# Optimization experiments

Measured on AMD Instinct MI355X. Metric: run time of the kernel, lower is better.

## Reference

```python
import jax, jax.numpy as jnp
import numpy as np

ALPHA = 2.0          # spikingjelly surrogate.ATan default alpha
V_THRESHOLD = 1.0    # IFNode default
# v_reset = 0.0 -> hard reset

@jax.custom_vjp
def atan_spike(x):
    # Heaviside forward, ATan surrogate backward
    return (x >= 0).astype(x.dtype)

def _atan_fwd(x):
    return atan_spike(x), x

def _atan_bwd(x, g):
    sg = (ALPHA / 2.0) / (1.0 + (jnp.pi / 2.0 * ALPHA * x) ** 2)
    return (g * sg,)

atan_spike.defvjp(_atan_fwd, _atan_bwd)

def if_node(x_seq):
    # x_seq: [T, B, D]; IF neuron: v += x; spike = H(v - th); hard reset to 0.
    # detach_reset=True -> stop_gradient on spike in the reset path.
    def step(v, xt):
        v = v + xt
        s = atan_spike(v - V_THRESHOLD)
        v = v * (1.0 - jax.lax.stop_gradient(s))
        return v, s
    v0 = jnp.zeros(x_seq.shape[1:], x_seq.dtype)
    _, spikes = jax.lax.scan(step, v0, x_seq)
    return spikes

def setup_inputs() -> dict:
    key = jax.random.key(0)
    k0, k1, k2, k3, k4 = jax.random.split(key, 5)
    B = 65536
    x = jax.random.normal(k0, (B, 1, 28, 28), dtype=jnp.float32)
    # Linear(28, 32) and Linear(32, 10) params (PyTorch layout: [out, in])
    W1 = jax.random.uniform(k1, (32, 28), jnp.float32, -1.0, 1.0) / np.sqrt(28.0).astype(np.float32)
    b1 = jax.random.uniform(k2, (32,), jnp.float32, -1.0, 1.0) / np.sqrt(28.0).astype(np.float32)
    W2 = jax.random.uniform(k3, (10, 32), jnp.float32, -1.0, 1.0) / np.sqrt(32.0).astype(np.float32)
    b2 = jax.random.uniform(k4, (10,), jnp.float32, -1.0, 1.0) / np.sqrt(32.0).astype(np.float32)
    return {"x": x, "W1": W1, "b1": b1, "W2": W2, "b2": b2}

def reference(x, W1, b1, W2, b2):
    # x: [B, 1, 28, 28] -> squeeze(1) -> [B, 28, 28] -> permute(2,0,1) -> [T=28, B, 28]
    xs = jnp.transpose(x[:, 0], (2, 0, 1))
    h1 = jnp.einsum('tbi,oi->tbo', xs, W1) + b1   # [28, B, 32]
    s1 = if_node(h1)
    h2 = jnp.einsum('tbi,oi->tbo', s1, W2) + b2   # [28, B, 10]
    s2 = if_node(h2)
    return s2.mean(axis=0)                         # [B, 10] firing rates
```

## Files before the change

kernel.cpp:

```cpp
#include <hip/hip_runtime.h>


#define SPB     8
#define THREADS 256

__global__ __launch_bounds__(THREADS, 4) void snn_if_kernel(
    const float* __restrict__ x,
    const float* __restrict__ W1,
    const float* __restrict__ b1,
    const float* __restrict__ W2,
    const float* __restrict__ b2,
    float* __restrict__ out,
    int B)
{
    __shared__ __align__(16) float xT[SPB][28][32];
    __shared__ float Tbl[1280];

    const int tid = threadIdx.x;
    const int o   = tid & 31;
    const int sl  = tid >> 5;
    const int S0  = blockIdx.x * SPB;
    const int nS  = (B - S0 < SPB) ? (B - S0) : SPB;

    const float4* x4 = (const float4*)x + (size_t)S0 * 196;
    for (int f = tid; f < nS * 196; f += THREADS) {
        int s  = f / 196;
        int r  = f - s * 196;
        int i  = r / 7;
        int tq = r - i * 7;
        float4 v = x4[f];
        int t0 = tq * 4;
        xT[s][t0 + 0][i] = v.x;
        xT[s][t0 + 1][i] = v.y;
        xT[s][t0 + 2][i] = v.z;
        xT[s][t0 + 3][i] = v.w;
    }

    for (int e = tid; e < 1280; e += THREADS) {
        int o2 = e % 10;
        int tn = e / 10;
        int n  = tn & 15;
        int k  = tn >> 4;
        float v = 0.f;
        if (n & 1) v += W2[o2 * 32 + 4 * k + 0];
        if (n & 2) v += W2[o2 * 32 + 4 * k + 1];
        if (n & 4) v += W2[o2 * 32 + 4 * k + 2];
        if (n & 8) v += W2[o2 * 32 + 4 * k + 3];
        Tbl[e] = v;
    }

    float w1r[28];
    {
        const float4* w4 = (const float4*)(W1 + o * 28);
        #pragma unroll
        for (int q = 0; q < 7; ++q) {
            float4 v = w4[q];
            w1r[4 * q + 0] = v.x; w1r[4 * q + 1] = v.y;
            w1r[4 * q + 2] = v.z; w1r[4 * q + 3] = v.w;
        }
    }
    const float b1o = b1[o];
    const float b2o = (o < 10) ? b2[o] : 0.f;

    __syncthreads();

    float v1 = 0.f, v2 = 0.f, cnt = 0.f;
    const float* xs = &xT[sl][0][0];

    for (int t = 0; t < 28; ++t) {
        const float4* xr = (const float4*)(xs + t * 32);
        float acc = 0.f;
        #pragma unroll
        for (int q = 0; q < 7; ++q) {
            float4 a = xr[q];
            acc = fmaf(w1r[4 * q + 0], a.x, acc);
            acc = fmaf(w1r[4 * q + 1], a.y, acc);
            acc = fmaf(w1r[4 * q + 2], a.z, acc);
            acc = fmaf(w1r[4 * q + 3], a.w, acc);
        }
        v1 += acc + b1o;
        bool sp = (v1 >= 1.0f);
        unsigned long long bal = __ballot(sp);
        if (sp) v1 = 0.0f;
        unsigned m = (unsigned)(bal >> (tid & 32));

        if (o < 10) {
            float acc2 = 0.f;
            #pragma unroll
            for (int k = 0; k < 8; ++k) {
                unsigned nib = (m >> (4 * k)) & 15u;
                acc2 += Tbl[k * 160 + nib * 10 + o];
            }
            v2 += acc2 + b2o;
            if (v2 >= 1.0f) { cnt += 1.0f; v2 = 0.0f; }
        }
    }

    if (o < 10 && (S0 + sl) < B) {
        out[(size_t)(S0 + sl) * 10 + o] = cnt / 28.0f;
    }
}

extern "C" void kernel_launch(void* const* d_in, const int* in_sizes, int n_in,
                              void* d_out, int out_size, void* d_ws, size_t ws_size,
                              hipStream_t stream) {
    const float* x  = (const float*)d_in[0];
    const float* W1 = (const float*)d_in[1];
    const float* b1 = (const float*)d_in[2];
    const float* W2 = (const float*)d_in[3];
    const float* b2 = (const float*)d_in[4];
    float* out = (float*)d_out;

    int B = in_sizes[0] / 784;
    int grid = (B + SPB - 1) / SPB;
    snn_if_kernel<<<grid, THREADS, 0, stream>>>(x, W1, b1, W2, b2, out, B);
}
```

Measured before the change: 388.8 us.

## Map one sample per thread with register-resident inputs and LDS membrane state

Changes the work split from one thread per hidden neuron (32 threads per sample) to one thread per sample. Each thread keeps a 4-timestep slice of its input in registers and loops over the 32 hidden neurons, streaming W1 rows through uniform loads and keeping the layer-1 membrane potentials in LDS. Spike masks are built arithmetically rather than with ballot, and layer 2 accumulates all 10 outputs per thread from the lookup table. This removes the shared-memory transpose and the ballot traffic, but it raises register pressure, leaves global input loads strided per thread, and cuts the block size to 128 with only 512 blocks, which may leave the GPU underfilled.

```diff
diff --git a/kernel.cpp b/kernel.cpp
--- a/kernel.cpp
+++ b/kernel.cpp
@@ -1,10 +1,9 @@
 #include <hip/hip_runtime.h>
 
 
-#define SPB     8
-#define THREADS 256
+#define THREADS 128
 
-__global__ __launch_bounds__(THREADS, 4) void snn_if_kernel(
+__global__ __launch_bounds__(THREADS, 1) void snn_if_kernel(
     const float* __restrict__ x,
     const float* __restrict__ W1,
     const float* __restrict__ b1,
@@ -13,28 +12,11 @@
     float* __restrict__ out,
     int B)
 {
-    __shared__ __align__(16) float xT[SPB][28][32];
     __shared__ float Tbl[1280];
+    __shared__ float v1L[32 * THREADS];
 
     const int tid = threadIdx.x;
-    const int o   = tid & 31;
-    const int sl  = tid >> 5;
-    const int S0  = blockIdx.x * SPB;
-    const int nS  = (B - S0 < SPB) ? (B - S0) : SPB;
-
-    const float4* x4 = (const float4*)x + (size_t)S0 * 196;
-    for (int f = tid; f < nS * 196; f += THREADS) {
-        int s  = f / 196;
-        int r  = f - s * 196;
-        int i  = r / 7;
-        int tq = r - i * 7;
-        float4 v = x4[f];
-        int t0 = tq * 4;
-        xT[s][t0 + 0][i] = v.x;
-        xT[s][t0 + 1][i] = v.y;
-        xT[s][t0 + 2][i] = v.z;
-        xT[s][t0 + 3][i] = v.w;
-    }
+    const int s   = blockIdx.x * THREADS + tid;
 
     for (int e = tid; e < 1280; e += THREADS) {
         int o2 = e % 10;
@@ -48,56 +30,110 @@
         if (n & 8) v += W2[o2 * 32 + 4 * k + 3];
         Tbl[e] = v;
     }
-
-    float w1r[28];
-    {
-        const float4* w4 = (const float4*)(W1 + o * 28);
-        #pragma unroll
-        for (int q = 0; q < 7; ++q) {
-            float4 v = w4[q];
-            w1r[4 * q + 0] = v.x; w1r[4 * q + 1] = v.y;
-            w1r[4 * q + 2] = v.z; w1r[4 * q + 3] = v.w;
-        }
-    }
-    const float b1o = b1[o];
-    const float b2o = (o < 10) ? b2[o] : 0.f;
-
     __syncthreads();
 
-    float v1 = 0.f, v2 = 0.f, cnt = 0.f;
-    const float* xs = &xT[sl][0][0];
+    if (s >= B) return;
 
-    for (int t = 0; t < 28; ++t) {
-        const float4* xr = (const float4*)(xs + t * 32);
-        float acc = 0.f;
+    const float* xs = x + (size_t)s * 784;
+
+    #pragma unroll
+    for (int o = 0; o < 32; ++o) v1L[o * THREADS + tid] = 0.f;
+
+    float v2[10], cnt[10], b2v[10];
+    #pragma unroll
+    for (int j = 0; j < 10; ++j) { v2[j] = 0.f; cnt[j] = 0.f; b2v[j] = b2[j]; }
+
+    float4 xq[28];
+    #pragma unroll
+    for (int i = 0; i < 28; ++i)
+        xq[i] = *reinterpret_cast<const float4*>(xs + i * 28);
+
+    float wA[28], wB[28];
+    #pragma unroll
+    for (int i = 0; i < 28; ++i) wA[i] = W1[i];
+
+    #pragma unroll 1
+    for (int t0 = 0; t0 < 28; t0 += 4) {
+        float mlo[4] = {0.f, 0.f, 0.f, 0.f};
+        float mhi[4] = {0.f, 0.f, 0.f, 0.f};
+
+        auto do_o = [&](int o, const float (&w)[28]) {
+            float a0 = 0.f, a1 = 0.f, a2 = 0.f, a3 = 0.f;
+            #pragma unroll
+            for (int i = 0; i < 28; ++i) {
+                const float wi = w[i];
+                a0 = fmaf(wi, xq[i].x, a0);
+                a1 = fmaf(wi, xq[i].y, a1);
+                a2 = fmaf(wi, xq[i].z, a2);
+                a3 = fmaf(wi, xq[i].w, a3);
+            }
+            const float b1o = b1[o];
+            const float pw  = (float)(1u << (o & 15));
+            float v1r = v1L[o * THREADS + tid];
+            const float av[4] = {a0, a1, a2, a3};
+            #pragma unroll
+            for (int tt = 0; tt < 4; ++tt) {
+                v1r = v1r + (av[tt] + b1o);
+                const bool sp = (v1r >= 1.0f);
+                const float spf = sp ? pw : 0.f;
+                if (o < 16) mlo[tt] += spf; else mhi[tt] += spf;
+                v1r = sp ? 0.0f : v1r;
+            }
+            v1L[o * THREADS + tid] = v1r;
+        };
+
+        #pragma unroll 1
+        for (int ob = 0; ob < 16; ++ob) {
+            const int o0 = 2 * ob, o1 = 2 * ob + 1;
+            #pragma unroll
+            for (int i = 0; i < 28; ++i) wB[i] = W1[o1 * 28 + i];
+            do_o(o0, wA);
+            const int onext = (o1 + 1) & 31;
+            #pragma unroll
+            for (int i = 0; i < 28; ++i) wA[i] = W1[onext * 28 + i];
+            do_o(o1, wB);
+        }
+
+        if (t0 + 4 < 28) {
+            #pragma unroll
+            for (int i = 0; i < 28; ++i)
+                xq[i] = *reinterpret_cast<const float4*>(xs + i * 28 + t0 + 4);
+        }
+
         #pragma unroll
-        for (int q = 0; q < 7; ++q) {
-            float4 a = xr[q];
-            acc = fmaf(w1r[4 * q + 0], a.x, acc);
-            acc = fmaf(w1r[4 * q + 1], a.y, acc);
-            acc = fmaf(w1r[4 * q + 2], a.z, acc);
-            acc = fmaf(w1r[4 * q + 3], a.w, acc);
-        }
-        v1 += acc + b1o;
-        bool sp = (v1 >= 1.0f);
-        unsigned long long bal = __ballot(sp);
-        if (sp) v1 = 0.0f;
-        unsigned m = (unsigned)(bal >> (tid & 32));
-
-        if (o < 10) {
-            float acc2 = 0.f;
+        for (int tt = 0; tt < 4; ++tt) {
+            const unsigned mask = (unsigned)mlo[tt] | ((unsigned)mhi[tt] << 16);
+            float acc2[10];
+            #pragma unroll
+            for (int j = 0; j < 10; ++j) acc2[j] = 0.f;
             #pragma unroll
             for (int k = 0; k < 8; ++k) {
-                unsigned nib = (m >> (4 * k)) & 15u;
-                acc2 += Tbl[k * 160 + nib * 10 + o];
+                const unsigned nib = (mask >> (4 * k)) & 15u;
+                const float2* p =
+                    reinterpret_cast<const float2*>(&Tbl[k * 160 + nib * 10]);
+                #pragma unroll
+                for (int j = 0; j < 5; ++j) {
+                    const float2 v = p[j];
+                    acc2[2 * j]     += v.x;
+                    acc2[2 * j + 1] += v.y;
+                }
             }
-            v2 += acc2 + b2o;
-            if (v2 >= 1.0f) { cnt += 1.0f; v2 = 0.0f; }
+            #pragma unroll
+            for (int o2 = 0; o2 < 10; ++o2) {
+                const float v2n = v2[o2] + (acc2[o2] + b2v[o2]);
+                const bool sp2 = (v2n >= 1.0f);
+                cnt[o2] += sp2 ? 1.0f : 0.0f;
+                v2[o2]   = sp2 ? 0.0f : v2n;
+            }
         }
     }
 
-    if (o < 10 && (S0 + sl) < B) {
-        out[(size_t)(S0 + sl) * 10 + o] = cnt / 28.0f;
+    #pragma unroll
+    for (int j = 0; j < 5; ++j) {
+        float2 r;
+        r.x = cnt[2 * j]     / 28.0f;
+        r.y = cnt[2 * j + 1] / 28.0f;
+        *reinterpret_cast<float2*>(out + (size_t)s * 10 + 2 * j) = r;
     }
 }
 
@@ -112,6 +148,6 @@
     float* out = (float*)d_out;
 
     int B = in_sizes[0] / 784;
-    int grid = (B + SPB - 1) / SPB;
+    int grid = (B + THREADS - 1) / THREADS;
     snn_if_kernel<<<grid, THREADS, 0, stream>>>(x, W1, b1, W2, b2, out, B);
 }
```

New measurement: 475.1 us. +22.2%, slower.

## Restructure SNN kernel into time-parallel phases with persistent blocks and global lookup table

Applied to the files above, without the earlier changes.

Splits the per-sample work into phases. In the first, threads map to timesteps and compute the layer-1 projections in parallel, with W1 read as wave-uniform scalars. The layer-1 IF recurrence then runs with ballot masks stored in shared memory, the layer-2 table lookups are done in parallel across timesteps using vectorized loads, and a short serial IF pass handles layer 2. Each block now loops over 16 groups of 8 samples, and the W2 lookup table is built once by a separate kernel into workspace. This removes the per-block table rebuild and the serial per-timestep matmul chain. In exchange it adds three block barriers per iteration and uses strided global loads of x without coalescing.

```diff
diff --git a/kernel.cpp b/kernel.cpp
--- a/kernel.cpp
+++ b/kernel.cpp
@@ -1,103 +1,163 @@
 #include <hip/hip_runtime.h>
 
 
-#define SPB     8
 #define THREADS 256
+#define SPI 8
+#define NITER 16
+#define SPB (SPI * NITER)
 
-__global__ __launch_bounds__(THREADS, 4) void snn_if_kernel(
+#define H1_TS 33
+#define H1_SS (32 * H1_TS)
+#define H2_TS 11
+#define H2_SS 309
+
+__global__ void build_tbl(const float* __restrict__ W2, float* __restrict__ Tbl)
+{
+    int e = blockIdx.x * blockDim.x + threadIdx.x;
+    if (e < 1536) {
+        int o2 = e % 12;
+        int tn = e / 12;
+        int n  = tn & 15;
+        int k  = tn >> 4;
+        float v = 0.f;
+        if (o2 < 10) {
+            if (n & 1) v += W2[o2 * 32 + 4 * k + 0];
+            if (n & 2) v += W2[o2 * 32 + 4 * k + 1];
+            if (n & 4) v += W2[o2 * 32 + 4 * k + 2];
+            if (n & 8) v += W2[o2 * 32 + 4 * k + 3];
+        }
+        Tbl[e] = v;
+    }
+}
+
+__global__ __launch_bounds__(THREADS, 2) void snn_if_kernel(
     const float* __restrict__ x,
     const float* __restrict__ W1,
     const float* __restrict__ b1,
     const float* __restrict__ W2,
     const float* __restrict__ b2,
+    const float* __restrict__ TblG,
     float* __restrict__ out,
     int B)
 {
-    __shared__ __align__(16) float xT[SPB][28][32];
-    __shared__ float Tbl[1280];
+    __shared__ __align__(16) float h1L[8 * H1_SS];
+    __shared__ __align__(16) float h2L[8 * H2_SS];
+    __shared__ unsigned maskL[8 * 33];
+    __shared__ __align__(16) float TblL[1536];
 
     const int tid = threadIdx.x;
-    const int o   = tid & 31;
-    const int sl  = tid >> 5;
-    const int S0  = blockIdx.x * SPB;
-    const int nS  = (B - S0 < SPB) ? (B - S0) : SPB;
+    const int s   = tid >> 5;
+    const int lo  = tid & 31;
 
-    const float4* x4 = (const float4*)x + (size_t)S0 * 196;
-    for (int f = tid; f < nS * 196; f += THREADS) {
-        int s  = f / 196;
-        int r  = f - s * 196;
-        int i  = r / 7;
-        int tq = r - i * 7;
-        float4 v = x4[f];
-        int t0 = tq * 4;
-        xT[s][t0 + 0][i] = v.x;
-        xT[s][t0 + 1][i] = v.y;
-        xT[s][t0 + 2][i] = v.z;
-        xT[s][t0 + 3][i] = v.w;
+    const float* tbl;
+    if (TblG != nullptr) {
+        tbl = TblG;
+    } else {
+        for (int e = tid; e < 1536; e += THREADS) {
+            int o2 = e % 12;
+            int tn = e / 12;
+            int n  = tn & 15;
+            int k  = tn >> 4;
+            float v = 0.f;
+            if (o2 < 10) {
+                if (n & 1) v += W2[o2 * 32 + 4 * k + 0];
+                if (n & 2) v += W2[o2 * 32 + 4 * k + 1];
+                if (n & 4) v += W2[o2 * 32 + 4 * k + 2];
+                if (n & 8) v += W2[o2 * 32 + 4 * k + 3];
+            }
+            TblL[e] = v;
+        }
+        tbl = TblL;
+        __syncthreads();
     }
 
-    for (int e = tid; e < 1280; e += THREADS) {
-        int o2 = e % 10;
-        int tn = e / 10;
-        int n  = tn & 15;
-        int k  = tn >> 4;
-        float v = 0.f;
-        if (n & 1) v += W2[o2 * 32 + 4 * k + 0];
-        if (n & 2) v += W2[o2 * 32 + 4 * k + 1];
-        if (n & 4) v += W2[o2 * 32 + 4 * k + 2];
-        if (n & 8) v += W2[o2 * 32 + 4 * k + 3];
-        Tbl[e] = v;
-    }
+    const float b1v = b1[lo];
+    const float b2v = (lo < 10) ? b2[lo] : 0.f;
+    const int   S0  = blockIdx.x * SPB;
 
-    float w1r[28];
-    {
-        const float4* w4 = (const float4*)(W1 + o * 28);
-        #pragma unroll
-        for (int q = 0; q < 7; ++q) {
-            float4 v = w4[q];
-            w1r[4 * q + 0] = v.x; w1r[4 * q + 1] = v.y;
-            w1r[4 * q + 2] = v.z; w1r[4 * q + 3] = v.w;
+    #pragma unroll 1
+    for (int it = 0; it < NITER; ++it) {
+        const int  sg    = S0 + it * SPI + s;
+        const bool valid = sg < B;
+        const int  sgc   = valid ? sg : (B - 1);
+
+        {
+            const int t = (lo < 28) ? lo : 27;
+            const float* xp = x + (size_t)sgc * 784 + t;
+            float xv[28];
+            #pragma unroll
+            for (int i = 0; i < 28; ++i) xv[i] = xp[i * 28];
+
+            float* hw = &h1L[s * H1_SS + lo * H1_TS];
+            #pragma unroll 2
+            for (int o = 0; o < 32; ++o) {
+                const int oro = __builtin_amdgcn_readfirstlane(o);
+                const float* wr = W1 + oro * 28;
+                float h = 0.f;
+                #pragma unroll
+                for (int i = 0; i < 28; ++i) h = fmaf(wr[i], xv[i], h);
+                hw[o] = h;
+            }
         }
-    }
-    const float b1o = b1[o];
-    const float b2o = (o < 10) ? b2[o] : 0.f;
+        __syncthreads();
 
-    __syncthreads();
+        {
+            const float* hp = &h1L[s * H1_SS + lo];
+            float hr[28];
+            #pragma unroll
+            for (int t = 0; t < 28; ++t) hr[t] = hp[t * H1_TS];
 
-    float v1 = 0.f, v2 = 0.f, cnt = 0.f;
-    const float* xs = &xT[sl][0][0];
+            float v = 0.f;
+            unsigned mym = 0u;
+            #pragma unroll
+            for (int t = 0; t < 28; ++t) {
+                v = v + (hr[t] + b1v);
+                const bool sp = (v >= 1.0f);
+                const unsigned long long bal = __ballot(sp);
+                if (lo == t) mym = (unsigned)(bal >> (tid & 32));
+                v = sp ? 0.0f : v;
+            }
+            if (lo < 28) maskL[s * 33 + lo] = mym;
+        }
+        __syncthreads();
 
-    for (int t = 0; t < 28; ++t) {
-        const float4* xr = (const float4*)(xs + t * 32);
-        float acc = 0.f;
-        #pragma unroll
-        for (int q = 0; q < 7; ++q) {
-            float4 a = xr[q];
-            acc = fmaf(w1r[4 * q + 0], a.x, acc);
-            acc = fmaf(w1r[4 * q + 1], a.y, acc);
-            acc = fmaf(w1r[4 * q + 2], a.z, acc);
-            acc = fmaf(w1r[4 * q + 3], a.w, acc);
-        }
-        v1 += acc + b1o;
-        bool sp = (v1 >= 1.0f);
-        unsigned long long bal = __ballot(sp);
-        if (sp) v1 = 0.0f;
-        unsigned m = (unsigned)(bal >> (tid & 32));
-
-        if (o < 10) {
-            float acc2 = 0.f;
+        {
+            const unsigned m = maskL[s * 33 + ((lo < 28) ? lo : 27)];
+            float a[10];
+            #pragma unroll
+            for (int j = 0; j < 10; ++j) a[j] = 0.f;
             #pragma unroll
             for (int k = 0; k < 8; ++k) {
-                unsigned nib = (m >> (4 * k)) & 15u;
-                acc2 += Tbl[k * 160 + nib * 10 + o];
+                const unsigned nib = (m >> (4 * k)) & 15u;
+                const float* p = tbl + (k * 192 + (int)nib * 12);
+                const float4 f0 = *(const float4*)(p);
+                const float4 f1 = *(const float4*)(p + 4);
+                const float2 f2 = *(const float2*)(p + 8);
+                a[0] += f0.x; a[1] += f0.y; a[2] += f0.z; a[3] += f0.w;
+                a[4] += f1.x; a[5] += f1.y; a[6] += f1.z; a[7] += f1.w;
+                a[8] += f2.x; a[9] += f2.y;
             }
-            v2 += acc2 + b2o;
-            if (v2 >= 1.0f) { cnt += 1.0f; v2 = 0.0f; }
+            if (lo < 28) {
+                float* hp = &h2L[s * H2_SS + lo * H2_TS];
+                #pragma unroll
+                for (int j = 0; j < 10; ++j) hp[j] = a[j];
+            }
         }
-    }
+        __syncthreads();
 
-    if (o < 10 && (S0 + sl) < B) {
-        out[(size_t)(S0 + sl) * 10 + o] = cnt / 28.0f;
+        if (lo < 10) {
+            float v2 = 0.f, cnt = 0.f;
+            const float* hp = &h2L[s * H2_SS + lo];
+            #pragma unroll
+            for (int t = 0; t < 28; ++t) {
+                const float h2 = hp[t * H2_TS];
+                const float vn = v2 + (h2 + b2v);
+                const bool sp = (vn >= 1.0f);
+                cnt += sp ? 1.0f : 0.0f;
+                v2 = sp ? 0.0f : vn;
+            }
+            if (valid) out[(size_t)sg * 10 + lo] = cnt / 28.0f;
+        }
     }
 }
 
@@ -112,6 +172,13 @@
     float* out = (float*)d_out;
 
     int B = in_sizes[0] / 784;
+
+    float* TblG = nullptr;
+    if (ws_size >= 1536 * sizeof(float)) {
+        TblG = (float*)d_ws;
+        build_tbl<<<6, 256, 0, stream>>>(W2, TblG);
+    }
+
     int grid = (B + SPB - 1) / SPB;
-    snn_if_kernel<<<grid, THREADS, 0, stream>>>(x, W1, b1, W2, b2, out, B);
+    snn_if_kernel<<<grid, THREADS, 0, stream>>>(x, W1, b1, W2, b2, TblG, out, B);
 }
```

New measurement: 361.0 us. 1.08x faster.
